# Performance work log

Measured on AMD Instinct MI355X. Metric: run time of the kernel, lower is better.

The kernel has to match this reference:

```python
import jax, jax.numpy as jnp
import numpy as np
import math

B, S, H = 1, 2048, 2048
NH, R = 16, 4            # num_heads, reduction_factor
KVH = NH // R            # reduced kv heads
HD = H // NH             # head_dim = 128
WIN = 128                # window_size
NEG = float('-inf')


def _masks(s):
    i = jnp.arange(s)[:, None]
    j = jnp.arange(s)[None, :]
    causal = jnp.where(j > i, NEG, 0.0).astype(jnp.float32)          # (S,S)
    local = jnp.where(jnp.abs(i - j) <= WIN // 2, 0.0, NEG).astype(jnp.float32)
    return causal, local


def setup_inputs() -> dict:
    key = jax.random.key(0)
    ks = jax.random.split(key, 7)
    sc = 1.0 / math.sqrt(H)
    return {
        'hidden_states': jax.random.normal(ks[0], (B, S, H), jnp.float32),
        'Wq': jax.random.normal(ks[1], (H, H), jnp.float32) * sc,
        'Wk': jax.random.normal(ks[2], (H, H // R), jnp.float32) * sc,
        'Wv': jax.random.normal(ks[3], (H, H // R), jnp.float32) * sc,
        'Wo': jax.random.normal(ks[4], (H, H), jnp.float32) * sc,
        'gate_w': jax.random.normal(ks[5], (H, 1), jnp.float32) * sc,
        'gate_b': jnp.zeros((1,), jnp.float32),
        'ln_g': jnp.ones((H,), jnp.float32),
        'ln_b': jnp.zeros((H,), jnp.float32),
    }


def _forward(hidden_states, Wq, Wk, Wv, Wo, gate_w, gate_b, ln_g, ln_b):
    b, s, _ = hidden_states.shape
    # gate: LayerNorm -> linear -> clamp -> sigmoid
    mu = jnp.mean(hidden_states, axis=-1, keepdims=True)
    var = jnp.var(hidden_states, axis=-1, keepdims=True)
    gi = (hidden_states - mu) * jax.lax.rsqrt(var + 1e-5) * ln_g + ln_b
    gates = jax.nn.sigmoid(jnp.clip(gi @ gate_w + gate_b, -10.0, 10.0))  # (b,s,1)

    q = (hidden_states @ Wq).reshape(b, s, NH, HD).transpose(0, 2, 1, 3)   # (b,NH,s,hd)
    k = (hidden_states @ Wk).reshape(b, s, KVH, HD).transpose(0, 2, 1, 3)  # (b,KVH,s,hd)
    v = (hidden_states @ Wv).reshape(b, s, KVH, HD).transpose(0, 2, 1, 3)
    # torch .repeat tiles the kv heads: head h uses kv head h % KVH
    k = jnp.tile(k, (1, R, 1, 1))
    v = jnp.tile(v, (1, R, 1, 1))

    scores = jnp.einsum('bhqd,bhkd->bhqk', q, k) / math.sqrt(HD)
    causal, local = _masks(s)
    local_p = jax.nn.softmax(scores + local, axis=-1)
    global_p = jax.nn.softmax(scores + causal, axis=-1)

    g = gates[:, None, :, :]  # (b,1,s,1): per-query gate, broadcast over heads/keys
    attn_probs = g * local_p + (1.0 - g) * global_p
    attn_out = jnp.einsum('bhqk,bhkd->bhqd', attn_probs, v)
    attn_out = attn_out.transpose(0, 2, 1, 3).reshape(b, s, H)
    output = attn_out @ Wo

    # regularization loss on gates (means over expanded tensor == per-token means)
    eps = 1e-5
    gf = gates
    gc = jnp.clip(gf, eps, 1.0 - eps)
    binary_reg = -0.1 * jnp.mean(gf * (1.0 - gf))
    entropy_reg = -0.01 * jnp.mean(gf * jnp.log(gc) + (1.0 - gf) * jnp.log(1.0 - gc))
    sparsity_reg = 0.1 * jnp.mean(gf)
    reg_loss = binary_reg + entropy_reg + sparsity_reg
    return output, reg_loss


def reference(hidden_states, Wq, Wk, Wv, Wo, gate_w, gate_b, ln_g, ln_b):
    return _forward(hidden_states, Wq, Wk, Wv, Wo, gate_w, gate_b, ln_g, ln_b)
```

## Files before the change

kernel.cpp:

```cpp
#include <hip/hip_runtime.h>
#include <hip/hip_bf16.h>
#include <math.h>

typedef __bf16 bf16_t;
typedef bf16_t bf16x8 __attribute__((ext_vector_type(8)));
typedef bf16_t bf16x4v __attribute__((ext_vector_type(4)));
typedef float f32x4 __attribute__((ext_vector_type(4)));

#define S_LEN 2048
#define HDIM 2048
#define QKV_LD 3072

__device__ __forceinline__ void gload_lds16(const bf16_t* g, bf16_t* l) {
  __builtin_amdgcn_global_load_lds(
      (const __attribute__((address_space(1))) unsigned int*)g,
      (__attribute__((address_space(3))) unsigned int*)l, 16, 0, 0);
}

__global__ __launch_bounds__(256) void ln_gate_cast_kernel(const float* __restrict__ hs,
                                                           const float* __restrict__ gw,
                                                           const float* __restrict__ gb,
                                                           const float* __restrict__ lng,
                                                           const float* __restrict__ lnb,
                                                           float* __restrict__ gates,
                                                           bf16_t* __restrict__ hsb) {
  __shared__ float red[256];
  int row = blockIdx.x, tid = threadIdx.x;
  const float* x = hs + (size_t)row * HDIM;
  bf16_t* y = hsb + (size_t)row * HDIM;
  float4 v0 = ((const float4*)x)[tid];
  float4 v1 = ((const float4*)x)[tid + 256];
  bf16x4v o;
  o[0] = (bf16_t)v0.x; o[1] = (bf16_t)v0.y; o[2] = (bf16_t)v0.z; o[3] = (bf16_t)v0.w;
  ((bf16x4v*)y)[tid] = o;
  o[0] = (bf16_t)v1.x; o[1] = (bf16_t)v1.y; o[2] = (bf16_t)v1.z; o[3] = (bf16_t)v1.w;
  ((bf16x4v*)y)[tid + 256] = o;
  float s = v0.x + v0.y + v0.z + v0.w + v1.x + v1.y + v1.z + v1.w;
  float ss = v0.x * v0.x + v0.y * v0.y + v0.z * v0.z + v0.w * v0.w +
             v1.x * v1.x + v1.y * v1.y + v1.z * v1.z + v1.w * v1.w;
  red[tid] = s; __syncthreads();
  for (int off = 128; off > 0; off >>= 1) { if (tid < off) red[tid] += red[tid + off]; __syncthreads(); }
  s = red[0]; __syncthreads();
  red[tid] = ss; __syncthreads();
  for (int off = 128; off > 0; off >>= 1) { if (tid < off) red[tid] += red[tid + off]; __syncthreads(); }
  ss = red[0]; __syncthreads();
  float mean = s * (1.f / HDIM);
  float var = ss * (1.f / HDIM) - mean * mean;
  float rstd = rsqrtf(var + 1e-5f);
  float dot = 0.f;
#pragma unroll
  for (int half = 0; half < 2; ++half) {
    int i = tid * 4 + half * 1024;
    float4 v = half ? v1 : v0;
    float4 g = *(const float4*)(lng + i);
    float4 b = *(const float4*)(lnb + i);
    float4 w = *(const float4*)(gw + i);
    dot += ((v.x - mean) * rstd * g.x + b.x) * w.x;
    dot += ((v.y - mean) * rstd * g.y + b.y) * w.y;
    dot += ((v.z - mean) * rstd * g.z + b.z) * w.z;
    dot += ((v.w - mean) * rstd * g.w + b.w) * w.w;
  }
  red[tid] = dot; __syncthreads();
  for (int off = 128; off > 0; off >>= 1) { if (tid < off) red[tid] += red[tid + off]; __syncthreads(); }
  if (tid == 0) {
    float gi = red[0] + gb[0];
    gi = fminf(10.f, fmaxf(-10.f, gi));
    gates[row] = 1.f / (1.f + __expf(-gi));
  }
}

__global__ __launch_bounds__(256) void wall_trans_kernel(const float* __restrict__ Wq,
                                                         const float* __restrict__ Wk,
                                                         const float* __restrict__ Wv,
                                                         const float* __restrict__ Wo,
                                                         bf16_t* __restrict__ wt,
                                                         bf16_t* __restrict__ wot) {
  __shared__ float tile[32][33];
  int bx = blockIdx.x, k0 = blockIdx.y * 32;
  const float* src; int N, n0; bf16_t* dst; int o0;
  if (bx < 64)      { src = Wq; N = 2048; n0 = bx * 32;        dst = wt;  o0 = n0; }
  else if (bx < 80) { src = Wk; N = 512;  n0 = (bx - 64) * 32; dst = wt;  o0 = 2048 + n0; }
  else if (bx < 96) { src = Wv; N = 512;  n0 = (bx - 80) * 32; dst = wt;  o0 = 2560 + n0; }
  else              { src = Wo; N = 2048; n0 = (bx - 96) * 32; dst = wot; o0 = n0; }
  int tx = threadIdx.x & 31, ty = threadIdx.x >> 5;
#pragma unroll
  for (int i = 0; i < 4; ++i)
    tile[ty + i * 8][tx] = src[(size_t)(k0 + ty + i * 8) * N + n0 + tx];
  __syncthreads();
#pragma unroll
  for (int i = 0; i < 4; ++i)
    dst[(size_t)(o0 + ty + i * 8) * 2048 + k0 + tx] = (bf16_t)tile[tx][ty + i * 8];
}

__global__ __launch_bounds__(256) void vtrans_kernel(const bf16_t* __restrict__ qkv,
                                                     bf16_t* __restrict__ vt) {
  __shared__ bf16_t tile[32][33];
  int v0 = blockIdx.x * 32, s0 = blockIdx.y * 32;
  int tx = threadIdx.x & 31, ty = threadIdx.x >> 5;
#pragma unroll
  for (int i = 0; i < 4; ++i)
    tile[ty + i * 8][tx] = qkv[(size_t)(s0 + ty + i * 8) * QKV_LD + 2560 + v0 + tx];
  __syncthreads();
#pragma unroll
  for (int i = 0; i < 4; ++i)
    vt[(size_t)(v0 + ty + i * 8) * S_LEN + s0 + tx] = tile[tx][ty + i * 8];
}

__global__ __launch_bounds__(256) void reg_loss_kernel(const float* __restrict__ gates,
                                                       float* __restrict__ out) {
  __shared__ float red[256];
  int tid = threadIdx.x;
  float sb = 0.f, se = 0.f, sg = 0.f;
  for (int i = tid; i < S_LEN; i += 256) {
    float g = gates[i];
    float gc = fminf(1.f - 1e-5f, fmaxf(1e-5f, g));
    sb += g * (1.f - g);
    se += g * logf(gc) + (1.f - g) * logf(1.f - gc);
    sg += g;
  }
  red[tid] = sb; __syncthreads();
  for (int off = 128; off > 0; off >>= 1) { if (tid < off) red[tid] += red[tid + off]; __syncthreads(); }
  sb = red[0]; __syncthreads();
  red[tid] = se; __syncthreads();
  for (int off = 128; off > 0; off >>= 1) { if (tid < off) red[tid] += red[tid + off]; __syncthreads(); }
  se = red[0]; __syncthreads();
  red[tid] = sg; __syncthreads();
  for (int off = 128; off > 0; off >>= 1) { if (tid < off) red[tid] += red[tid + off]; __syncthreads(); }
  if (tid == 0) {
    const float inv = 1.f / (float)S_LEN;
    float reg = -0.1f * (sb * inv) - 0.01f * (se * inv) + 0.1f * (red[0] * inv);
    out[0] = reg;
  }
}

template <typename OutT>
__global__ __launch_bounds__(512) void gemm_bt_kernel(const bf16_t* __restrict__ A,
                                                      const bf16_t* __restrict__ Bt,
                                                      OutT* __restrict__ C,
                                                      int M, int N, int K) {
  __shared__ bf16_t As[2][128][32];
  __shared__ bf16_t Bs[2][128][32];
  int tid = threadIdx.x;
  int lane = tid & 63, wave = tid >> 6;
  int wr = wave >> 2, wc = wave & 3;
  int m0 = blockIdx.y * 128, n0 = blockIdx.x * 128;
  int lrow = lane & 15, lhi = lane >> 4;

  int srow = wave * 16 + (lane >> 2);
  int scol = (lane & 3) * 8;
  const bf16_t* Ag = A + (size_t)(m0 + srow) * K + scol;
  const bf16_t* Bg = Bt + (size_t)(n0 + srow) * K + scol;

  f32x4 acc[4][2];
#pragma unroll
  for (int a = 0; a < 4; ++a)
#pragma unroll
    for (int b = 0; b < 2; ++b)
#pragma unroll
      for (int r = 0; r < 4; ++r) acc[a][b][r] = 0.f;

  gload_lds16(Ag, &As[0][wave * 16][0]);
  gload_lds16(Bg, &Bs[0][wave * 16][0]);
  __syncthreads();

  int cur = 0;
  for (int k0 = 0; k0 < K; k0 += 32) {
    int nxt = cur ^ 1;
    if (k0 + 32 < K) {
      gload_lds16(Ag + k0 + 32, &As[nxt][wave * 16][0]);
      gload_lds16(Bg + k0 + 32, &Bs[nxt][wave * 16][0]);
    }
    bf16x8 af[4], bfr[2];
#pragma unroll
    for (int a = 0; a < 4; ++a)
      af[a] = *(const bf16x8*)(&As[cur][wr * 64 + a * 16 + lrow][lhi * 8]);
#pragma unroll
    for (int b = 0; b < 2; ++b)
      bfr[b] = *(const bf16x8*)(&Bs[cur][wc * 32 + b * 16 + lrow][lhi * 8]);
    __builtin_amdgcn_s_setprio(1);
#pragma unroll
    for (int a = 0; a < 4; ++a)
#pragma unroll
      for (int b = 0; b < 2; ++b)
        acc[a][b] = __builtin_amdgcn_mfma_f32_16x16x32_bf16(af[a], bfr[b], acc[a][b], 0, 0, 0);
    __builtin_amdgcn_s_setprio(0);
    __syncthreads();
    cur = nxt;
  }
#pragma unroll
  for (int a = 0; a < 4; ++a)
#pragma unroll
    for (int b = 0; b < 2; ++b)
#pragma unroll
      for (int r = 0; r < 4; ++r) {
        int row = m0 + wr * 64 + a * 16 + lhi * 4 + r;
        int col = n0 + wc * 32 + b * 16 + lrow;
        C[(size_t)row * N + col] = (OutT)acc[a][b][r];
      }
}

__global__ __launch_bounds__(256, 2) void attn_kernel(const bf16_t* __restrict__ QKV,
                                                      const bf16_t* __restrict__ VTg,
                                                      const float* __restrict__ gates,
                                                      bf16_t* __restrict__ out) {
  __shared__ bf16_t Ks[2][64][128];
  __shared__ bf16_t Vt[2][128][64];
  __shared__ bf16_t Pw[4][16][72];

  int b = blockIdx.x;
  int h = b & 15;
  int t5 = b >> 4;
  int c = (t5 < 16) ? (31 - t5) : (t5 - 16);
  int q0c = c * 64;
  int tid = threadIdx.x;
  int lane = tid & 63, w = tid >> 6;
  int lrow = lane & 15, lhi = lane >> 4;
  int q0w = q0c + w * 16;
  int hk = h & 3;
  const bf16_t* Qp = QKV + h * 128;
  const bf16_t* Kp = QKV + 2048 + hk * 128;
  const bf16_t* Vt_g = VTg + (size_t)hk * 128 * S_LEN;

  bf16x8 aq[4];
#pragma unroll
  for (int ks = 0; ks < 4; ++ks)
    aq[ks] = *(const bf16x8*)(Qp + (size_t)(q0w + lrow) * QKV_LD + ks * 32 + lhi * 8);

  float lg[4], ll[4];
  f32x4 og[8], ol[8];
#pragma unroll
  for (int r = 0; r < 4; ++r) { lg[r] = ll[r] = 0.f; }
#pragma unroll
  for (int d = 0; d < 8; ++d)
#pragma unroll
    for (int r = 0; r < 4; ++r) { og[d][r] = 0.f; ol[d][r] = 0.f; }

  const float NEGINF = -__builtin_inff();
  const float scl = 0.08838834764831845f;
  const float MFIX = 8.0f;
  int kend = q0c + 128;
  if (kend > S_LEN) kend = S_LEN;
  int nt = kend >> 6;

  int kr = tid >> 4, c16 = tid & 15;
  int vr = tid >> 3, c8 = tid & 7;

  {
    bf16x8 kreg[4], vreg[4];
#pragma unroll
    for (int i = 0; i < 4; ++i)
      kreg[i] = *(const bf16x8*)(Kp + (size_t)(kr + i * 16) * QKV_LD + c16 * 8);
#pragma unroll
    for (int i = 0; i < 4; ++i)
      vreg[i] = *(const bf16x8*)(Vt_g + (size_t)(vr + i * 32) * S_LEN + c8 * 8);
#pragma unroll
    for (int i = 0; i < 4; ++i) {
      int rr = kr + i * 16;
      *(bf16x8*)(&Ks[0][rr][(c16 ^ (rr & 7)) * 8]) = kreg[i];
    }
#pragma unroll
    for (int i = 0; i < 4; ++i) {
      int rr = vr + i * 32;
      *(bf16x8*)(&Vt[0][rr][(c8 ^ (rr & 7)) * 8]) = vreg[i];
    }
  }
  __syncthreads();

  for (int ti = 0; ti < nt; ++ti) {
    int k0 = ti << 6;
    int bufc = ti & 1, bufn = bufc ^ 1;
    bool more = (ti + 1 < nt);

    bf16x8 kreg[4], vreg[4];
    if (more) {
      int k0n = k0 + 64;
#pragma unroll
      for (int i = 0; i < 4; ++i)
        kreg[i] = *(const bf16x8*)(Kp + (size_t)(k0n + kr + i * 16) * QKV_LD + c16 * 8);
#pragma unroll
      for (int i = 0; i < 4; ++i)
        vreg[i] = *(const bf16x8*)(Vt_g + (size_t)(vr + i * 32) * S_LEN + k0n + c8 * 8);
    }

    f32x4 sc[4];
#pragma unroll
    for (int t = 0; t < 4; ++t) {
#pragma unroll
      for (int r = 0; r < 4; ++r) sc[t][r] = 0.f;
    }
#pragma unroll
    for (int t = 0; t < 4; ++t) {
      int n = t * 16 + lrow;
      int swz = n & 7;
#pragma unroll
      for (int ks = 0; ks < 4; ++ks) {
        bf16x8 bk = *(const bf16x8*)(&Ks[bufc][n][((ks * 4 + lhi) ^ swz) * 8]);
        sc[t] = __builtin_amdgcn_mfma_f32_16x16x32_bf16(aq[ks], bk, sc[t], 0, 0, 0);
      }
    }

    bool g_act = (k0 <= q0w + 15);
    bool g_full = (k0 + 63 <= q0w);
    bool l_act = (k0 + 63 >= q0w - 64) && (k0 <= q0w + 79);

    if (g_act) {
#pragma unroll
      for (int r = 0; r < 4; ++r) {
        int i = q0w + lhi * 4 + r;
        float v0, v1, v2, v3;
        if (g_full) {
          v0 = sc[0][r] * scl; v1 = sc[1][r] * scl;
          v2 = sc[2][r] * scl; v3 = sc[3][r] * scl;
        } else {
          int j = k0 + lrow;
          v0 = (j > i) ? NEGINF : sc[0][r] * scl;
          v1 = (j + 16 > i) ? NEGINF : sc[1][r] * scl;
          v2 = (j + 32 > i) ? NEGINF : sc[2][r] * scl;
          v3 = (j + 48 > i) ? NEGINF : sc[3][r] * scl;
        }
        float p0 = __expf(v0 - MFIX), p1 = __expf(v1 - MFIX);
        float p2 = __expf(v2 - MFIX), p3 = __expf(v3 - MFIX);
        int pr = lhi * 4 + r;
        Pw[w][pr][lrow] = (bf16_t)p0;
        Pw[w][pr][16 + lrow] = (bf16_t)p1;
        Pw[w][pr][32 + lrow] = (bf16_t)p2;
        Pw[w][pr][48 + lrow] = (bf16_t)p3;
        lg[r] += (p0 + p1) + (p2 + p3);
      }
      bf16x8 ap0 = *(const bf16x8*)(&Pw[w][lrow][lhi * 8]);
      bf16x8 ap1 = *(const bf16x8*)(&Pw[w][lrow][32 + lhi * 8]);
#pragma unroll
      for (int d = 0; d < 8; ++d) {
        int drow = d * 16 + lrow;
        int swz = drow & 7;
        bf16x8 bv0 = *(const bf16x8*)(&Vt[bufc][drow][(lhi ^ swz) * 8]);
        bf16x8 bv1 = *(const bf16x8*)(&Vt[bufc][drow][((4 + lhi) ^ swz) * 8]);
        og[d] = __builtin_amdgcn_mfma_f32_16x16x32_bf16(ap0, bv0, og[d], 0, 0, 0);
        og[d] = __builtin_amdgcn_mfma_f32_16x16x32_bf16(ap1, bv1, og[d], 0, 0, 0);
      }
    }

    if (l_act) {
#pragma unroll
      for (int r = 0; r < 4; ++r) {
        int i = q0w + lhi * 4 + r;
        int j = k0 + lrow;
        int d0 = i - j, d1 = d0 - 16, d2 = d0 - 32, d3 = d0 - 48;
        float v0 = (d0 > 64 || d0 < -64) ? NEGINF : sc[0][r] * scl;
        float v1 = (d1 > 64 || d1 < -64) ? NEGINF : sc[1][r] * scl;
        float v2 = (d2 > 64 || d2 < -64) ? NEGINF : sc[2][r] * scl;
        float v3 = (d3 > 64 || d3 < -64) ? NEGINF : sc[3][r] * scl;
        float p0 = __expf(v0 - MFIX), p1 = __expf(v1 - MFIX);
        float p2 = __expf(v2 - MFIX), p3 = __expf(v3 - MFIX);
        int pr = lhi * 4 + r;
        Pw[w][pr][lrow] = (bf16_t)p0;
        Pw[w][pr][16 + lrow] = (bf16_t)p1;
        Pw[w][pr][32 + lrow] = (bf16_t)p2;
        Pw[w][pr][48 + lrow] = (bf16_t)p3;
        ll[r] += (p0 + p1) + (p2 + p3);
      }
      bf16x8 ap0 = *(const bf16x8*)(&Pw[w][lrow][lhi * 8]);
      bf16x8 ap1 = *(const bf16x8*)(&Pw[w][lrow][32 + lhi * 8]);
#pragma unroll
      for (int d = 0; d < 8; ++d) {
        int drow = d * 16 + lrow;
        int swz = drow & 7;
        bf16x8 bv0 = *(const bf16x8*)(&Vt[bufc][drow][(lhi ^ swz) * 8]);
        bf16x8 bv1 = *(const bf16x8*)(&Vt[bufc][drow][((4 + lhi) ^ swz) * 8]);
        ol[d] = __builtin_amdgcn_mfma_f32_16x16x32_bf16(ap0, bv0, ol[d], 0, 0, 0);
        ol[d] = __builtin_amdgcn_mfma_f32_16x16x32_bf16(ap1, bv1, ol[d], 0, 0, 0);
      }
    }

    if (more) {
#pragma unroll
      for (int i = 0; i < 4; ++i) {
        int rr = kr + i * 16;
        *(bf16x8*)(&Ks[bufn][rr][(c16 ^ (rr & 7)) * 8]) = kreg[i];
      }
#pragma unroll
      for (int i = 0; i < 4; ++i) {
        int rr = vr + i * 32;
        *(bf16x8*)(&Vt[bufn][rr][(c8 ^ (rr & 7)) * 8]) = vreg[i];
      }
    }
    __syncthreads();
  }

#pragma unroll
  for (int r = 0; r < 4; ++r) {
#pragma unroll
    for (int m = 1; m < 16; m <<= 1) {
      lg[r] += __shfl_xor(lg[r], m, 64);
      ll[r] += __shfl_xor(ll[r], m, 64);
    }
  }

#pragma unroll
  for (int r = 0; r < 4; ++r) {
    int i = q0w + lhi * 4 + r;
    float gv = gates[i];
    float il = 1.f / ll[r], ig = 1.f / lg[r];
#pragma unroll
    for (int d = 0; d < 8; ++d)
      out[(size_t)i * HDIM + h * 128 + d * 16 + lrow] =
          (bf16_t)(gv * ol[d][r] * il + (1.f - gv) * og[d][r] * ig);
  }
}

extern "C" void kernel_launch(void* const* d_in, const int* in_sizes, int n_in,
                              void* d_out, int out_size, void* d_ws, size_t ws_size,
                              hipStream_t stream) {
  const float* hs  = (const float*)d_in[0];
  const float* Wq  = (const float*)d_in[1];
  const float* Wk  = (const float*)d_in[2];
  const float* Wv  = (const float*)d_in[3];
  const float* Wo  = (const float*)d_in[4];
  const float* gw  = (const float*)d_in[5];
  const float* gb  = (const float*)d_in[6];
  const float* lng = (const float*)d_in[7];
  const float* lnb = (const float*)d_in[8];
  float* out = (float*)d_out;

  char* ws = (char*)d_ws;
  bf16_t* hsb   = (bf16_t*)(ws);
  bf16_t* wt    = (bf16_t*)(ws + 8388608);
  bf16_t* wot   = (bf16_t*)(ws + 20971520);
  bf16_t* qkv   = (bf16_t*)(ws + 29360128);
  bf16_t* ao    = (bf16_t*)(ws + 41943040);
  float*  gates = (float*)(ws + 50331648);
  bf16_t* vtb   = (bf16_t*)(ws + 50339840);

  ln_gate_cast_kernel<<<2048, 256, 0, stream>>>(hs, gw, gb, lng, lnb, gates, hsb);
  wall_trans_kernel<<<dim3(160, 64), 256, 0, stream>>>(Wq, Wk, Wv, Wo, wt, wot);
  reg_loss_kernel<<<1, 256, 0, stream>>>(gates, out + (size_t)4194304);

  gemm_bt_kernel<bf16_t><<<dim3(24, 16), 512, 0, stream>>>(hsb, wt, qkv, 2048, 3072, 2048);

  vtrans_kernel<<<dim3(16, 64), 256, 0, stream>>>(qkv, vtb);

  attn_kernel<<<dim3(512), 256, 0, stream>>>(qkv, vtb, gates, ao);

  gemm_bt_kernel<float><<<dim3(16, 16), 512, 0, stream>>>(ao, wot, out, 2048, 2048, 2048);
}
```

Baseline: 174.2 us.

## Single-buffer attention K/V tiles for higher occupancy and swizzle GEMM block order

The attention kernel drops LDS double buffering for K and V, which roughly halves shared memory per block. It raises launch bounds to 3 blocks per CU and adds an extra barrier before overwriting the tiles. The GEMM kernel remaps the block index with a stride-8 swizzle so neighbouring blocks spread differently across the output, aiming at better cache locality across XCDs. The extra barrier serialises the LDS store with compute, and the tighter register budget may cause spills.

After: 208.4 us. 1.2x slower.

```diff
diff --git a/kernel.cpp b/kernel.cpp
--- a/kernel.cpp
+++ b/kernel.cpp
@@ -143,7 +143,13 @@
   int tid = threadIdx.x;
   int lane = tid & 63, wave = tid >> 6;
   int wr = wave >> 2, wc = wave & 3;
-  int m0 = blockIdx.y * 128, n0 = blockIdx.x * 128;
+
+  int lid = blockIdx.y * gridDim.x + blockIdx.x;
+  int total = gridDim.x * gridDim.y;
+  int qq = total >> 3;
+  int swzid = (lid & 7) * qq + (lid >> 3);
+  int m0 = (swzid / gridDim.x) * 128, n0 = (swzid % gridDim.x) * 128;
+
   int lrow = lane & 15, lhi = lane >> 4;
 
   int srow = wave * 16 + (lane >> 2);
@@ -199,12 +205,12 @@
       }
 }
 
-__global__ __launch_bounds__(256, 2) void attn_kernel(const bf16_t* __restrict__ QKV,
+__global__ __launch_bounds__(256, 3) void attn_kernel(const bf16_t* __restrict__ QKV,
                                                       const bf16_t* __restrict__ VTg,
                                                       const float* __restrict__ gates,
                                                       bf16_t* __restrict__ out) {
-  __shared__ bf16_t Ks[2][64][128];
-  __shared__ bf16_t Vt[2][128][64];
+  __shared__ bf16_t Ks[64][128];
+  __shared__ bf16_t Vt[128][64];
   __shared__ bf16_t Pw[4][16][72];
 
   int b = blockIdx.x;
@@ -256,19 +262,18 @@
 #pragma unroll
     for (int i = 0; i < 4; ++i) {
       int rr = kr + i * 16;
-      *(bf16x8*)(&Ks[0][rr][(c16 ^ (rr & 7)) * 8]) = kreg[i];
+      *(bf16x8*)(&Ks[rr][(c16 ^ (rr & 7)) * 8]) = kreg[i];
     }
 #pragma unroll
     for (int i = 0; i < 4; ++i) {
       int rr = vr + i * 32;
-      *(bf16x8*)(&Vt[0][rr][(c8 ^ (rr & 7)) * 8]) = vreg[i];
+      *(bf16x8*)(&Vt[rr][(c8 ^ (rr & 7)) * 8]) = vreg[i];
     }
   }
   __syncthreads();
 
   for (int ti = 0; ti < nt; ++ti) {
     int k0 = ti << 6;
-    int bufc = ti & 1, bufn = bufc ^ 1;
     bool more = (ti + 1 < nt);
 
     bf16x8 kreg[4], vreg[4];
@@ -294,7 +299,7 @@
       int swz = n & 7;
 #pragma unroll
       for (int ks = 0; ks < 4; ++ks) {
-        bf16x8 bk = *(const bf16x8*)(&Ks[bufc][n][((ks * 4 + lhi) ^ swz) * 8]);
+        bf16x8 bk = *(const bf16x8*)(&Ks[n][((ks * 4 + lhi) ^ swz) * 8]);
         sc[t] = __builtin_amdgcn_mfma_f32_16x16x32_bf16(aq[ks], bk, sc[t], 0, 0, 0);
       }
     }
@@ -333,8 +338,8 @@
       for (int d = 0; d < 8; ++d) {
         int drow = d * 16 + lrow;
         int swz = drow & 7;
-        bf16x8 bv0 = *(const bf16x8*)(&Vt[bufc][drow][(lhi ^ swz) * 8]);
-        bf16x8 bv1 = *(const bf16x8*)(&Vt[bufc][drow][((4 + lhi) ^ swz) * 8]);
+        bf16x8 bv0 = *(const bf16x8*)(&Vt[drow][(lhi ^ swz) * 8]);
+        bf16x8 bv1 = *(const bf16x8*)(&Vt[drow][((4 + lhi) ^ swz) * 8]);
         og[d] = __builtin_amdgcn_mfma_f32_16x16x32_bf16(ap0, bv0, og[d], 0, 0, 0);
         og[d] = __builtin_amdgcn_mfma_f32_16x16x32_bf16(ap1, bv1, og[d], 0, 0, 0);
       }
@@ -365,23 +370,24 @@
       for (int d = 0; d < 8; ++d) {
         int drow = d * 16 + lrow;
         int swz = drow & 7;
-        bf16x8 bv0 = *(const bf16x8*)(&Vt[bufc][drow][(lhi ^ swz) * 8]);
-        bf16x8 bv1 = *(const bf16x8*)(&Vt[bufc][drow][((4 + lhi) ^ swz) * 8]);
+        bf16x8 bv0 = *(const bf16x8*)(&Vt[drow][(lhi ^ swz) * 8]);
+        bf16x8 bv1 = *(const bf16x8*)(&Vt[drow][((4 + lhi) ^ swz) * 8]);
         ol[d] = __builtin_amdgcn_mfma_f32_16x16x32_bf16(ap0, bv0, ol[d], 0, 0, 0);
         ol[d] = __builtin_amdgcn_mfma_f32_16x16x32_bf16(ap1, bv1, ol[d], 0, 0, 0);
       }
     }
 
+    __syncthreads();
     if (more) {
 #pragma unroll
       for (int i = 0; i < 4; ++i) {
         int rr = kr + i * 16;
-        *(bf16x8*)(&Ks[bufn][rr][(c16 ^ (rr & 7)) * 8]) = kreg[i];
+        *(bf16x8*)(&Ks[rr][(c16 ^ (rr & 7)) * 8]) = kreg[i];
       }
 #pragma unroll
       for (int i = 0; i < 4; ++i) {
         int rr = vr + i * 32;
-        *(bf16x8*)(&Vt[bufn][rr][(c8 ^ (rr & 7)) * 8]) = vreg[i];
+        *(bf16x8*)(&Vt[rr][(c8 ^ (rr & 7)) * 8]) = vreg[i];
       }
     }
     __syncthreads();
```
